# Kernel optimization log

Measured on AMD Instinct MI355X. Metric: run time of the kernel, lower is better.

## Reference

```python
import jax, jax.numpy as jnp
import numpy as np

NUM_Q_HEADS = 32
NUM_KV_HEADS = 8
HEAD_DIM = 128
ROPE_THETA = 10000.0
Q_SIZE = NUM_Q_HEADS * HEAD_DIM      # 4096
KV_SIZE = NUM_KV_HEADS * HEAD_DIM    # 1024


def _apply_rope_neox(x, positions, theta=ROPE_THETA):
    # x: [T, H, D]; neox-style rotate-halves RoPE
    T, H, D = x.shape
    half = D // 2
    inv_freq = 1.0 / (theta ** (jnp.arange(half, dtype=jnp.float32) / half))
    freqs = positions.astype(jnp.float32)[:, None] * inv_freq[None, :]  # [T, half]
    cos = jnp.cos(freqs)[:, None, :]  # [T, 1, half]
    sin = jnp.sin(freqs)[:, None, :]
    x1, x2 = x[..., :half], x[..., half:]
    return jnp.concatenate([x1 * cos - x2 * sin, x2 * cos + x1 * sin], axis=-1).astype(x.dtype)


def setup_inputs() -> dict:
    key = jax.random.key(0)
    k1, k2, k3 = jax.random.split(key, 3)
    T, E = 8192, 4096
    hidden_states = jax.random.normal(k1, (T, E), dtype=jnp.float32) * 0.02
    positions = jnp.arange(T, dtype=jnp.int32)
    w_qkv = jax.random.normal(k2, (E, Q_SIZE + 2 * KV_SIZE), dtype=jnp.float32) * 0.02
    w_o = jax.random.normal(k3, (Q_SIZE, E), dtype=jnp.float32) * 0.02
    return {"hidden_states": hidden_states, "positions": positions, "w_qkv": w_qkv, "w_o": w_o}


def reference(hidden_states, positions, w_qkv, w_o):
    T = hidden_states.shape[0]
    qkv = hidden_states @ w_qkv                              # [T, 6144]
    q = qkv[:, :Q_SIZE].reshape(T, NUM_Q_HEADS, HEAD_DIM)
    k = qkv[:, Q_SIZE:Q_SIZE + KV_SIZE].reshape(T, NUM_KV_HEADS, HEAD_DIM)
    v = qkv[:, Q_SIZE + KV_SIZE:]                            # [T, KV_SIZE] (unused by stub)
    q = _apply_rope_neox(q, positions)
    k = _apply_rope_neox(k, positions)
    # Attention is stubbed in the source (randn_like(q)); we use the RoPE'd q
    # as the deterministic stand-in so the pipeline stays reproducible.
    attn_output = q.reshape(T, Q_SIZE)
    output = attn_output @ w_o                               # [T, 4096]
    return output
```

## Files before the change

kernel.cpp:

```cpp
#include <hip/hip_runtime.h>
#include <hip/hip_bf16.h>
#include <stdint.h>

#define T_DIM 8192
#define E_DIM 4096
#define NQH   32
#define HD    128
#define QSZ   (NQH * HD)
#define QKV_COLS 6144

typedef unsigned short u16;
typedef __attribute__((ext_vector_type(8))) short   bf16x8;
typedef __attribute__((ext_vector_type(4))) float   f32x4;
typedef __attribute__((ext_vector_type(4))) unsigned short u16x4;

__device__ __forceinline__ u16 f2bf(float f) {
    uint32_t u = __float_as_uint(f);
    u += 0x7fffu + ((u >> 16) & 1u);
    return (u16)(u >> 16);
}
__device__ __forceinline__ float bf2f(u16 u) {
    return __uint_as_float(((uint32_t)u) << 16);
}

__device__ __forceinline__ void gload_lds16(u16* lds, const u16* g) {
    __builtin_amdgcn_global_load_lds(
        (const __attribute__((address_space(1))) uint32_t*)g,
        (__attribute__((address_space(3))) uint32_t*)lds,
        16, 0, 0);
}

__global__ void convert_f32_bf16(const float* __restrict__ in, u16* __restrict__ out, size_t n4) {
    size_t i = (size_t)blockIdx.x * blockDim.x + threadIdx.x;
    size_t stride = (size_t)gridDim.x * blockDim.x;
    for (; i < n4; i += stride) {
        float4 v = ((const float4*)in)[i];
        u16x4 o;
        o.x = f2bf(v.x); o.y = f2bf(v.y); o.z = f2bf(v.z); o.w = f2bf(v.w);
        ((u16x4*)out)[i] = o;
    }
}

__global__ void transpose_conv(const float* __restrict__ W, u16* __restrict__ Wt,
                               int K, int N, int ldW, int colOff) {
    __shared__ float tile[32][33];
    const int tx = threadIdx.x, ty = threadIdx.y;
    const int n0 = blockIdx.x * 32, k0 = blockIdx.y * 32;
#pragma unroll
    for (int j = 0; j < 4; ++j) {
        int k = k0 + ty + j * 8;
        tile[ty + j * 8][tx] = W[(size_t)k * ldW + colOff + n0 + tx];
    }
    __syncthreads();
#pragma unroll
    for (int j = 0; j < 4; ++j) {
        int n = n0 + ty + j * 8;
        Wt[(size_t)n * K + k0 + tx] = f2bf(tile[tx][ty + j * 8]);
    }
}

__global__ void rope_kernel(u16* __restrict__ Q, const int* __restrict__ pos) {
    const size_t total = (size_t)T_DIM * (QSZ / 2);
    size_t stride = (size_t)gridDim.x * blockDim.x;
    for (size_t idx = (size_t)blockIdx.x * blockDim.x + threadIdx.x; idx < total; idx += stride) {
        int t = (int)(idx >> 11);
        int r = (int)(idx & 2047);
        int h = r >> 6;
        int d = r & 63;
        size_t base = (size_t)t * QSZ + h * HD;
        float x1 = bf2f(Q[base + d]);
        float x2 = bf2f(Q[base + d + 64]);
        float inv = powf(10000.0f, -(float)d * (1.0f / 64.0f));
        float fr  = (float)pos[t] * inv;
        float s, c;
        sincosf(fr, &s, &c);
        Q[base + d]      = f2bf(x1 * c - x2 * s);
        Q[base + d + 64] = f2bf(x2 * c + x1 * s);
    }
}

__device__ __forceinline__ void store_out(u16* p, float v)  { *p = f2bf(v); }
__device__ __forceinline__ void store_out(float* p, float v){ *p = v; }

#define BARS()    do { __builtin_amdgcn_sched_barrier(0); __builtin_amdgcn_s_barrier(); } while (0)
#define BARSPUB() do { __builtin_amdgcn_sched_barrier(0); __builtin_amdgcn_s_barrier(); \
                       __builtin_amdgcn_sched_barrier(0); } while (0)
#define VMC(N) asm volatile("s_waitcnt vmcnt(%0)" :: "n"(N) : "memory")

#define STG_A(buf, h, kOff) do { \
    const u16* s_ = sA + (size_t)(h) * 128 * K + (kOff); \
    u16* d_ = dL + (buf) * 32768 + (h) * 8192; \
    gload_lds16(d_, s_); gload_lds16(d_ + 4096, s_ + (size_t)64 * K); } while (0)
#define STG_B(buf, h, kOff) do { \
    const u16* s_ = sB + (size_t)(h) * 128 * K + (kOff); \
    u16* d_ = dL + 16384 + (buf) * 32768 + (h) * 8192; \
    gload_lds16(d_, s_); gload_lds16(d_ + 4096, s_ + (size_t)64 * K); } while (0)

#define RD_A(buf, miBase, d0, d1) do { _Pragma("unroll") \
    for (int m = 0; m < 4; ++m) { \
        const u16* p_ = lds + (buf) * 32768 + wm * 8192 + ((miBase) + m) * 1024 + aRow; \
        d0[m] = *(const bf16x8*)(p_ + cOf0); \
        d1[m] = *(const bf16x8*)(p_ + cOf1); } } while (0)
#define RD_B(buf, niBase, d0, d1) do { _Pragma("unroll") \
    for (int n = 0; n < 2; ++n) { \
        const u16* p_ = lds + (buf) * 32768 + 16384 + (wn >> 1) * 8192 + \
                        ((wn & 1) * 64 + ((niBase) + n) * 16) * 64 + aRow; \
        d0[n] = *(const bf16x8*)(p_ + cOf0); \
        d1[n] = *(const bf16x8*)(p_ + cOf1); } } while (0)

#define MM(miBase, niBase, A0, A1, B0, B1) do { \
    __builtin_amdgcn_s_setprio(1); \
    _Pragma("unroll") for (int m = 0; m < 4; ++m) \
    _Pragma("unroll") for (int n = 0; n < 2; ++n) { \
        acc[(miBase) + m][(niBase) + n] = __builtin_amdgcn_mfma_f32_16x16x32_bf16( \
            A0[m], B0[n], acc[(miBase) + m][(niBase) + n], 0, 0, 0); \
        acc[(miBase) + m][(niBase) + n] = __builtin_amdgcn_mfma_f32_16x16x32_bf16( \
            A1[m], B1[n], acc[(miBase) + m][(niBase) + n], 0, 0, 0); } \
    __builtin_amdgcn_s_setprio(0); } while (0)

template <typename OutT>
__global__ __launch_bounds__(512, 2) void gemm256(const u16* __restrict__ A,
                                                  const u16* __restrict__ Bt,
                                                  OutT* __restrict__ C,
                                                  int M, int N, int K) {
    __shared__ u16 lds[65536];
    const int tid  = threadIdx.x;
    const int lane = tid & 63;
    const int wid  = tid >> 6;
    const int wm = wid >> 2;
    const int wn = wid & 3;
    const int lr  = lane & 15;
    const int kq  = lane >> 4;
    const int lr7 = lr & 7;
    const int aRow = lr * 64;
    const int cOf0 = ((kq) ^ lr7) << 3;
    const int cOf1 = ((4 + kq) ^ lr7) << 3;

    const int nwg = gridDim.x;
    const int cpx = nwg >> 3;
    const int bid = blockIdx.x;
    const int swz = (bid & 7) * cpx + (bid >> 3);
    const int numM = M >> 8;
    const size_t rowBase = (size_t)(swz % numM) << 8;
    const size_t colBase = (size_t)(swz / numM) << 8;

    const int r0 = tid >> 3;
    const int cS = (((tid & 7) ^ (r0 & 7)) << 3);
    const u16* sA = A  + (rowBase + r0) * (size_t)K + cS;
    const u16* sB = Bt + (colBase + r0) * (size_t)K + cS;
    u16* dL = &lds[0] + tid * 8;

    f32x4 acc[8][4];
#pragma unroll
    for (int i = 0; i < 8; ++i)
#pragma unroll
        for (int j = 0; j < 4; ++j)
            acc[i][j] = (f32x4){0.f, 0.f, 0.f, 0.f};

    bf16x8 a0K0[4], a0K1[4], a4K0[4], a4K1[4];
    bf16x8 b01eK0[2], b01eK1[2], b01oK0[2], b01oK1[2], b23K0[2], b23K1[2];

    STG_A(0, 0, 0); STG_A(0, 1, 0); STG_B(0, 0, 0); STG_B(0, 1, 0);
    STG_B(1, 0, 64); STG_B(1, 1, 64);
    VMC(4);
    BARSPUB();
    RD_A(0, 0, a0K0, a0K1);
    RD_B(0, 0, b01eK0, b01eK1);

    const int nIter = K >> 7;
    for (int it = 0; it < nIter; ++it) {
        const int k1  = ((it << 1) + 1) << 6;
        const int kt2 = ((it << 1) + 2) << 6;
        const int kt3 = ((it << 1) + 3) << 6;
        const int k2c = (kt2 <= K - 64) ? kt2 : 0;
        const int k3c = (kt3 <= K - 64) ? kt3 : 0;

        STG_A(1, 0, k1);
        BARS();
        RD_B(0, 2, b23K0, b23K1);
        MM(0, 0, a0K0, a0K1, b01eK0, b01eK1);
        STG_A(1, 1, k1);
        BARS();
        RD_A(0, 4, a4K0, a4K1);
        MM(0, 2, a0K0, a0K1, b23K0, b23K1);
        STG_B(0, 0, k2c);
        BARS();
        MM(4, 2, a4K0, a4K1, b23K0, b23K1);
        STG_B(0, 1, k2c);
        VMC(4);
        BARSPUB();
        RD_A(1, 0, a0K0, a0K1);
        RD_B(1, 0, b01oK0, b01oK1);
        MM(4, 0, a4K0, a4K1, b01eK0, b01eK1);
        STG_A(0, 0, k2c);
        BARS();
        RD_B(1, 2, b23K0, b23K1);
        MM(0, 0, a0K0, a0K1, b01oK0, b01oK1);
        STG_A(0, 1, k2c);
        BARS();
        RD_A(1, 4, a4K0, a4K1);
        MM(0, 2, a0K0, a0K1, b23K0, b23K1);
        STG_B(1, 0, k3c);
        BARS();
        MM(4, 2, a4K0, a4K1, b23K0, b23K1);
        STG_B(1, 1, k3c);
        VMC(4);
        BARSPUB();
        RD_A(0, 0, a0K0, a0K1);
        RD_B(0, 0, b01eK0, b01eK1);
        MM(4, 0, a4K0, a4K1, b01oK0, b01oK1);
    }

    asm volatile("s_waitcnt vmcnt(0)" ::: "memory");

#pragma unroll
    for (int mi = 0; mi < 8; ++mi)
#pragma unroll
        for (int ni = 0; ni < 4; ++ni)
#pragma unroll
            for (int r = 0; r < 4; ++r) {
                size_t row = rowBase + wm * 128 + mi * 16 + (kq << 2) + r;
                size_t col = colBase + wn * 64 + ni * 16 + lr;
                store_out(&C[row * (size_t)N + col], acc[mi][ni][r]);
            }
}

extern "C" void kernel_launch(void* const* d_in, const int* in_sizes, int n_in,
                              void* d_out, int out_size, void* d_ws, size_t ws_size,
                              hipStream_t stream) {
    const float* hidden    = (const float*)d_in[0];
    const int*   positions = (const int*)d_in[1];
    const float* w_qkv     = (const float*)d_in[2];
    const float* w_o       = (const float*)d_in[3];
    float* out = (float*)d_out;

    u16* Hb  = (u16*)d_ws;
    u16* WqT = Hb  + (size_t)T_DIM * E_DIM;
    u16* WoT = WqT + (size_t)QSZ * E_DIM;
    u16* Qb  = WoT + (size_t)E_DIM * QSZ;

    convert_f32_bf16<<<2048, 256, 0, stream>>>(hidden, Hb, (size_t)T_DIM * E_DIM / 4);

    dim3 tb(32, 8);
    transpose_conv<<<dim3(QSZ / 32, E_DIM / 32), tb, 0, stream>>>(w_qkv, WqT, E_DIM, QSZ, QKV_COLS, 0);
    transpose_conv<<<dim3(E_DIM / 32, QSZ / 32), tb, 0, stream>>>(w_o,   WoT, QSZ,   E_DIM, E_DIM,  0);

    gemm256<u16><<<dim3((T_DIM / 256) * (QSZ / 256)), 512, 0, stream>>>(Hb, WqT, Qb, T_DIM, QSZ, E_DIM);

    rope_kernel<<<4096, 256, 0, stream>>>(Qb, positions);

    gemm256<float><<<dim3((T_DIM / 256) * (E_DIM / 256)), 512, 0, stream>>>(Qb, WoT, out, T_DIM, E_DIM, QSZ);
}
```

Before: 605.7 us.

## Fuse RoPE into QKV GEMM epilogue and restructure LDS pipeline

Removes the standalone RoPE kernel by applying the rotation in the epilogue of the Q projection GEMM. Each wave's column mapping is remapped so a thread holds both d and d+64 elements of a head. The main loop is also rewritten into a HALF_ITER macro that stages a full next k-tile at once and changes the LDS read order and waits. This drops one full read-write pass over the Q buffer, but changes the memory pipelining (VMC(0) waits) and may alter overlap or register pressure.

```diff
diff --git a/kernel.cpp b/kernel.cpp
--- a/kernel.cpp
+++ b/kernel.cpp
@@ -59,26 +59,6 @@
     }
 }
 
-__global__ void rope_kernel(u16* __restrict__ Q, const int* __restrict__ pos) {
-    const size_t total = (size_t)T_DIM * (QSZ / 2);
-    size_t stride = (size_t)gridDim.x * blockDim.x;
-    for (size_t idx = (size_t)blockIdx.x * blockDim.x + threadIdx.x; idx < total; idx += stride) {
-        int t = (int)(idx >> 11);
-        int r = (int)(idx & 2047);
-        int h = r >> 6;
-        int d = r & 63;
-        size_t base = (size_t)t * QSZ + h * HD;
-        float x1 = bf2f(Q[base + d]);
-        float x2 = bf2f(Q[base + d + 64]);
-        float inv = powf(10000.0f, -(float)d * (1.0f / 64.0f));
-        float fr  = (float)pos[t] * inv;
-        float s, c;
-        sincosf(fr, &s, &c);
-        Q[base + d]      = f2bf(x1 * c - x2 * s);
-        Q[base + d + 64] = f2bf(x2 * c + x1 * s);
-    }
-}
-
 __device__ __forceinline__ void store_out(u16* p, float v)  { *p = f2bf(v); }
 __device__ __forceinline__ void store_out(float* p, float v){ *p = v; }
 
@@ -96,17 +76,22 @@
     u16* d_ = dL + 16384 + (buf) * 32768 + (h) * 8192; \
     gload_lds16(d_, s_); gload_lds16(d_ + 4096, s_ + (size_t)64 * K); } while (0)
 
-#define RD_A(buf, miBase, d0, d1) do { _Pragma("unroll") \
-    for (int m = 0; m < 4; ++m) { \
-        const u16* p_ = lds + (buf) * 32768 + wm * 8192 + ((miBase) + m) * 1024 + aRow; \
-        d0[m] = *(const bf16x8*)(p_ + cOf0); \
-        d1[m] = *(const bf16x8*)(p_ + cOf1); } } while (0)
-#define RD_B(buf, niBase, d0, d1) do { _Pragma("unroll") \
-    for (int n = 0; n < 2; ++n) { \
-        const u16* p_ = lds + (buf) * 32768 + 16384 + (wn >> 1) * 8192 + \
-                        ((wn & 1) * 64 + ((niBase) + n) * 16) * 64 + aRow; \
-        d0[n] = *(const bf16x8*)(p_ + cOf0); \
-        d1[n] = *(const bf16x8*)(p_ + cOf1); } } while (0)
+#define RD_A0(buf, mi, ix) do { \
+    const u16* p_ = lds + (buf) * 32768 + wm * 8192 + (mi) * 1024 + lr * 64; \
+    a0K0[ix] = *(const bf16x8*)(p_ + cOf0); \
+    a0K1[ix] = *(const bf16x8*)(p_ + cOf1); } while (0)
+#define RD_A4(buf, mi, ix) do { \
+    const u16* p_ = lds + (buf) * 32768 + wm * 8192 + (mi) * 1024 + lr * 64; \
+    a4K0[ix] = *(const bf16x8*)(p_ + cOf0); \
+    a4K1[ix] = *(const bf16x8*)(p_ + cOf1); } while (0)
+
+#define RD_B2(buf, ni0, d0, d1) do { _Pragma("unroll") \
+    for (int n_ = 0; n_ < 2; ++n_) { \
+        const int ni_ = (ni0) + n_; \
+        const u16* p_ = lds + (buf) * 32768 + 16384 + (ni_ >> 1) * 8192 + \
+                        ((ni_ & 1) * 64 + wn * 16 + lr) * 64; \
+        d0[n_] = *(const bf16x8*)(p_ + cOf0); \
+        d1[n_] = *(const bf16x8*)(p_ + cOf1); } } while (0)
 
 #define MM(miBase, niBase, A0, A1, B0, B1) do { \
     __builtin_amdgcn_s_setprio(1); \
@@ -118,10 +103,37 @@
             A1[m], B1[n], acc[(miBase) + m][(niBase) + n], 0, 0, 0); } \
     __builtin_amdgcn_s_setprio(0); } while (0)
 
-template <typename OutT>
+#define HALF_ITER(bufT, bufN, BC0, BC1, BN0, BN1, kN)                          \
+  do {                                                                         \
+                                                                       \
+    STG_A(bufN, 0, kN); STG_A(bufN, 1, kN);                                    \
+    STG_B(bufN, 0, kN); STG_B(bufN, 1, kN);                                    \
+    BARS();                                                                    \
+    RD_B2(bufT, 2, b23K0, b23K1);                                              \
+    RD_A4(bufT, 4, 0);                                                         \
+    MM(0, 0, a0K0, a0K1, BC0, BC1);                                            \
+                                                                       \
+    BARS();                                                                    \
+    RD_A4(bufT, 5, 1); RD_A4(bufT, 6, 2); RD_A4(bufT, 7, 3);                   \
+    MM(0, 2, a0K0, a0K1, b23K0, b23K1);                                        \
+                                                       \
+    VMC(4);                                                                    \
+    BARSPUB();                                                                 \
+    RD_A0(bufN, 0, 0); RD_A0(bufN, 1, 1); RD_A0(bufN, 2, 2);                   \
+    MM(4, 2, a4K0, a4K1, b23K0, b23K1);                                        \
+                                                       \
+    VMC(0);                                                                    \
+    BARSPUB();                                                                 \
+    RD_A0(bufN, 3, 3);                                                         \
+    RD_B2(bufN, 0, BN0, BN1);                                                  \
+    MM(4, 0, a4K0, a4K1, BC0, BC1);                                            \
+  } while (0)
+
+template <typename OutT, bool ROPE>
 __global__ __launch_bounds__(512, 2) void gemm256(const u16* __restrict__ A,
                                                   const u16* __restrict__ Bt,
                                                   OutT* __restrict__ C,
+                                                  const int* __restrict__ pos,
                                                   int M, int N, int K) {
     __shared__ u16 lds[65536];
     const int tid  = threadIdx.x;
@@ -132,7 +144,6 @@
     const int lr  = lane & 15;
     const int kq  = lane >> 4;
     const int lr7 = lr & 7;
-    const int aRow = lr * 64;
     const int cOf0 = ((kq) ^ lr7) << 3;
     const int cOf1 = ((4 + kq) ^ lr7) << 3;
 
@@ -161,68 +172,53 @@
     bf16x8 b01eK0[2], b01eK1[2], b01oK0[2], b01oK1[2], b23K0[2], b23K1[2];
 
     STG_A(0, 0, 0); STG_A(0, 1, 0); STG_B(0, 0, 0); STG_B(0, 1, 0);
-    STG_B(1, 0, 64); STG_B(1, 1, 64);
-    VMC(4);
+    VMC(0);
     BARSPUB();
-    RD_A(0, 0, a0K0, a0K1);
-    RD_B(0, 0, b01eK0, b01eK1);
+    RD_A0(0, 0, 0); RD_A0(0, 1, 1); RD_A0(0, 2, 2); RD_A0(0, 3, 3);
+    RD_B2(0, 0, b01eK0, b01eK1);
 
     const int nIter = K >> 7;
     for (int it = 0; it < nIter; ++it) {
-        const int k1  = ((it << 1) + 1) << 6;
-        const int kt2 = ((it << 1) + 2) << 6;
-        const int kt3 = ((it << 1) + 3) << 6;
-        const int k2c = (kt2 <= K - 64) ? kt2 : 0;
-        const int k3c = (kt3 <= K - 64) ? kt3 : 0;
-
-        STG_A(1, 0, k1);
-        BARS();
-        RD_B(0, 2, b23K0, b23K1);
-        MM(0, 0, a0K0, a0K1, b01eK0, b01eK1);
-        STG_A(1, 1, k1);
-        BARS();
-        RD_A(0, 4, a4K0, a4K1);
-        MM(0, 2, a0K0, a0K1, b23K0, b23K1);
-        STG_B(0, 0, k2c);
-        BARS();
-        MM(4, 2, a4K0, a4K1, b23K0, b23K1);
-        STG_B(0, 1, k2c);
-        VMC(4);
-        BARSPUB();
-        RD_A(1, 0, a0K0, a0K1);
-        RD_B(1, 0, b01oK0, b01oK1);
-        MM(4, 0, a4K0, a4K1, b01eK0, b01eK1);
-        STG_A(0, 0, k2c);
-        BARS();
-        RD_B(1, 2, b23K0, b23K1);
-        MM(0, 0, a0K0, a0K1, b01oK0, b01oK1);
-        STG_A(0, 1, k2c);
-        BARS();
-        RD_A(1, 4, a4K0, a4K1);
-        MM(0, 2, a0K0, a0K1, b23K0, b23K1);
-        STG_B(1, 0, k3c);
-        BARS();
-        MM(4, 2, a4K0, a4K1, b23K0, b23K1);
-        STG_B(1, 1, k3c);
-        VMC(4);
-        BARSPUB();
-        RD_A(0, 0, a0K0, a0K1);
-        RD_B(0, 0, b01eK0, b01eK1);
-        MM(4, 0, a4K0, a4K1, b01oK0, b01oK1);
-    }
-
-    asm volatile("s_waitcnt vmcnt(0)" ::: "memory");
-
-#pragma unroll
-    for (int mi = 0; mi < 8; ++mi)
-#pragma unroll
-        for (int ni = 0; ni < 4; ++ni)
+        const int kOdd  = ((it << 1) + 1) << 6;
+        int kEven = ((it << 1) + 2) << 6;
+        if (kEven >= K) kEven = 0;
+        HALF_ITER(0, 1, b01eK0, b01eK1, b01oK0, b01oK1, kOdd);
+        HALF_ITER(1, 0, b01oK0, b01oK1, b01eK0, b01eK1, kEven);
+    }
+    VMC(0);
+
+    if constexpr (ROPE) {
+        const float d   = (float)(wn * 16 + lr);
+        const float inv = powf(10000.0f, -d * (1.0f / 64.0f));
+#pragma unroll
+        for (int mi = 0; mi < 8; ++mi)
 #pragma unroll
             for (int r = 0; r < 4; ++r) {
                 size_t row = rowBase + wm * 128 + mi * 16 + (kq << 2) + r;
-                size_t col = colBase + wn * 64 + ni * 16 + lr;
-                store_out(&C[row * (size_t)N + col], acc[mi][ni][r]);
+                float fr = (float)pos[row] * inv;
+                float s, c;
+                sincosf(fr, &s, &c);
+#pragma unroll
+                for (int hp = 0; hp < 2; ++hp) {
+                    float x1 = acc[mi][hp * 2 + 0][r];
+                    float x2 = acc[mi][hp * 2 + 1][r];
+                    size_t c1 = colBase + hp * 128 + wn * 16 + lr;
+                    C[row * (size_t)N + c1]      = f2bf(x1 * c - x2 * s);
+                    C[row * (size_t)N + c1 + 64] = f2bf(x2 * c + x1 * s);
+                }
             }
+    } else {
+#pragma unroll
+        for (int mi = 0; mi < 8; ++mi)
+#pragma unroll
+            for (int ni = 0; ni < 4; ++ni)
+#pragma unroll
+                for (int r = 0; r < 4; ++r) {
+                    size_t row = rowBase + wm * 128 + mi * 16 + (kq << 2) + r;
+                    size_t col = colBase + ni * 64 + wn * 16 + lr;
+                    store_out(&C[row * (size_t)N + col], acc[mi][ni][r]);
+                }
+    }
 }
 
 extern "C" void kernel_launch(void* const* d_in, const int* in_sizes, int n_in,
@@ -245,9 +241,9 @@
     transpose_conv<<<dim3(QSZ / 32, E_DIM / 32), tb, 0, stream>>>(w_qkv, WqT, E_DIM, QSZ, QKV_COLS, 0);
     transpose_conv<<<dim3(E_DIM / 32, QSZ / 32), tb, 0, stream>>>(w_o,   WoT, QSZ,   E_DIM, E_DIM,  0);
 
-    gemm256<u16><<<dim3((T_DIM / 256) * (QSZ / 256)), 512, 0, stream>>>(Hb, WqT, Qb, T_DIM, QSZ, E_DIM);
-
-    rope_kernel<<<4096, 256, 0, stream>>>(Qb, positions);
-
-    gemm256<float><<<dim3((T_DIM / 256) * (E_DIM / 256)), 512, 0, stream>>>(Qb, WoT, out, T_DIM, E_DIM, QSZ);
-}
+    gemm256<u16, true><<<dim3((T_DIM / 256) * (QSZ / 256)), 512, 0, stream>>>(
+        Hb, WqT, Qb, positions, T_DIM, QSZ, E_DIM);
+
+    gemm256<float, false><<<dim3((T_DIM / 256) * (E_DIM / 256)), 512, 0, stream>>>(
+        Qb, WoT, out, nullptr, T_DIM, E_DIM, QSZ);
+}
```

After: 1.049 ms. +73.3%, slower.

## Fuse RoPE into QKV GEMM epilogue by remapping B-tile column ownership

Applied to the files above, without the earlier changes.

Removes the standalone RoPE kernel and applies the rotation in the first GEMM's epilogue. To make this possible, the mapping of B-tile columns to waves is changed so that each thread holds both halves (d and d+64) of a head in its accumulators. The second GEMM's store indexing is updated to match. This saves a full read-modify-write pass over the 8192x4096 bf16 Q buffer and one kernel launch, at the cost of sincos/pow work in the epilogue and a possibly different LDS read pattern.

```diff
diff --git a/kernel.cpp b/kernel.cpp
--- a/kernel.cpp
+++ b/kernel.cpp
@@ -59,26 +59,6 @@
     }
 }
 
-__global__ void rope_kernel(u16* __restrict__ Q, const int* __restrict__ pos) {
-    const size_t total = (size_t)T_DIM * (QSZ / 2);
-    size_t stride = (size_t)gridDim.x * blockDim.x;
-    for (size_t idx = (size_t)blockIdx.x * blockDim.x + threadIdx.x; idx < total; idx += stride) {
-        int t = (int)(idx >> 11);
-        int r = (int)(idx & 2047);
-        int h = r >> 6;
-        int d = r & 63;
-        size_t base = (size_t)t * QSZ + h * HD;
-        float x1 = bf2f(Q[base + d]);
-        float x2 = bf2f(Q[base + d + 64]);
-        float inv = powf(10000.0f, -(float)d * (1.0f / 64.0f));
-        float fr  = (float)pos[t] * inv;
-        float s, c;
-        sincosf(fr, &s, &c);
-        Q[base + d]      = f2bf(x1 * c - x2 * s);
-        Q[base + d + 64] = f2bf(x2 * c + x1 * s);
-    }
-}
-
 __device__ __forceinline__ void store_out(u16* p, float v)  { *p = f2bf(v); }
 __device__ __forceinline__ void store_out(float* p, float v){ *p = v; }
 
@@ -103,8 +83,9 @@
         d1[m] = *(const bf16x8*)(p_ + cOf1); } } while (0)
 #define RD_B(buf, niBase, d0, d1) do { _Pragma("unroll") \
     for (int n = 0; n < 2; ++n) { \
-        const u16* p_ = lds + (buf) * 32768 + 16384 + (wn >> 1) * 8192 + \
-                        ((wn & 1) * 64 + ((niBase) + n) * 16) * 64 + aRow; \
+        const int ni_ = (niBase) + n; \
+        const u16* p_ = lds + (buf) * 32768 + 16384 + (ni_ >> 1) * 8192 + \
+                        ((ni_ & 1) * 64 + wn * 16) * 64 + aRow; \
         d0[n] = *(const bf16x8*)(p_ + cOf0); \
         d1[n] = *(const bf16x8*)(p_ + cOf1); } } while (0)
 
@@ -118,10 +99,11 @@
             A1[m], B1[n], acc[(miBase) + m][(niBase) + n], 0, 0, 0); } \
     __builtin_amdgcn_s_setprio(0); } while (0)
 
-template <typename OutT>
+template <typename OutT, bool ROPE>
 __global__ __launch_bounds__(512, 2) void gemm256(const u16* __restrict__ A,
                                                   const u16* __restrict__ Bt,
                                                   OutT* __restrict__ C,
+                                                  const int* __restrict__ pos,
                                                   int M, int N, int K) {
     __shared__ u16 lds[65536];
     const int tid  = threadIdx.x;
@@ -213,16 +195,38 @@
 
     asm volatile("s_waitcnt vmcnt(0)" ::: "memory");
 
-#pragma unroll
-    for (int mi = 0; mi < 8; ++mi)
-#pragma unroll
-        for (int ni = 0; ni < 4; ++ni)
+    if constexpr (ROPE) {
+        const float d   = (float)(wn * 16 + lr);
+        const float inv = powf(10000.0f, -d * (1.0f / 64.0f));
+#pragma unroll
+        for (int mi = 0; mi < 8; ++mi)
 #pragma unroll
             for (int r = 0; r < 4; ++r) {
                 size_t row = rowBase + wm * 128 + mi * 16 + (kq << 2) + r;
-                size_t col = colBase + wn * 64 + ni * 16 + lr;
-                store_out(&C[row * (size_t)N + col], acc[mi][ni][r]);
+                float fr = (float)pos[row] * inv;
+                float s, c;
+                sincosf(fr, &s, &c);
+#pragma unroll
+                for (int hp = 0; hp < 2; ++hp) {
+                    float x1 = acc[mi][hp * 2 + 0][r];
+                    float x2 = acc[mi][hp * 2 + 1][r];
+                    size_t c1 = colBase + hp * 128 + wn * 16 + lr;
+                    C[row * (size_t)N + c1]      = f2bf(x1 * c - x2 * s);
+                    C[row * (size_t)N + c1 + 64] = f2bf(x2 * c + x1 * s);
+                }
             }
+    } else {
+#pragma unroll
+        for (int mi = 0; mi < 8; ++mi)
+#pragma unroll
+            for (int ni = 0; ni < 4; ++ni)
+#pragma unroll
+                for (int r = 0; r < 4; ++r) {
+                    size_t row = rowBase + wm * 128 + mi * 16 + (kq << 2) + r;
+                    size_t col = colBase + ni * 64 + wn * 16 + lr;
+                    store_out(&C[row * (size_t)N + col], acc[mi][ni][r]);
+                }
+    }
 }
 
 extern "C" void kernel_launch(void* const* d_in, const int* in_sizes, int n_in,
@@ -245,9 +249,9 @@
     transpose_conv<<<dim3(QSZ / 32, E_DIM / 32), tb, 0, stream>>>(w_qkv, WqT, E_DIM, QSZ, QKV_COLS, 0);
     transpose_conv<<<dim3(E_DIM / 32, QSZ / 32), tb, 0, stream>>>(w_o,   WoT, QSZ,   E_DIM, E_DIM,  0);
 
-    gemm256<u16><<<dim3((T_DIM / 256) * (QSZ / 256)), 512, 0, stream>>>(Hb, WqT, Qb, T_DIM, QSZ, E_DIM);
-
-    rope_kernel<<<4096, 256, 0, stream>>>(Qb, positions);
-
-    gemm256<float><<<dim3((T_DIM / 256) * (E_DIM / 256)), 512, 0, stream>>>(Qb, WoT, out, T_DIM, E_DIM, QSZ);
-}
+    gemm256<u16, true><<<dim3((T_DIM / 256) * (QSZ / 256)), 512, 0, stream>>>(
+        Hb, WqT, Qb, positions, T_DIM, QSZ, E_DIM);
+
+    gemm256<float, false><<<dim3((T_DIM / 256) * (E_DIM / 256)), 512, 0, stream>>>(
+        Qb, WoT, out, nullptr, T_DIM, E_DIM, QSZ);
+}
```

Result: slower. 753.7 us (+24.4%).
